# Kernel optimization log

Hardware: AMD Instinct MI355X
Metric: run time of the kernel (lower is better)

## Reference

```python
import jax, jax.numpy as jnp
import numpy as np

N = 100000      # num_entities
D = 128         # embedding_dim
H = 128         # hidden_layer_size
R2 = 100        # num_relations * 2 (with inverse relations)
B = 4           # num_bases
E = 400000      # num_edges


def setup_inputs() -> dict:
    key = jax.random.key(0)
    ks = jax.random.split(key, 12)
    s = 0.1
    return {
        "edge_index": jax.random.randint(ks[0], (2, E), 0, N),
        "edge_type": jax.random.randint(ks[1], (E,), 0, R2),
        "entity_embedding": jax.random.normal(ks[2], (N, D), jnp.float32) * s,
        "entity_embedding_bias": jnp.zeros((1, D), jnp.float32),
        "bases1": jax.random.normal(ks[3], (B, D, H), jnp.float32) * s,
        "comp1": jax.random.normal(ks[4], (R2, B), jnp.float32) * s,
        "root1": jax.random.normal(ks[5], (D, H), jnp.float32) * s,
        "bias1": jnp.zeros((H,), jnp.float32),
        "bases2": jax.random.normal(ks[6], (B, H, D), jnp.float32) * s,
        "comp2": jax.random.normal(ks[7], (R2, B), jnp.float32) * s,
        "root2": jax.random.normal(ks[8], (H, D), jnp.float32) * s,
        "bias2": jnp.zeros((D,), jnp.float32),
        "rel_emb": jax.random.normal(ks[9], (R2, D), jnp.float32) * s,
    }


def _rgcn_layer(x, bases, comp, root, bias, src, dst, et, norm):
    # gather source features and project through all bases: [E, B, out]
    xb = jnp.einsum('ei,bio->ebo', x[src], bases)
    # relation-specific basis mix per edge: [E, out]
    msg = jnp.einsum('eb,ebo->eo', comp[et], xb) * norm[:, None]
    # scatter-add aggregate to destination nodes
    agg = jax.ops.segment_sum(msg, dst, num_segments=N)
    return agg + x @ root + bias


def reference(edge_index, edge_type, entity_embedding, entity_embedding_bias,
              bases1, comp1, root1, bias1, bases2, comp2, root2, bias2, rel_emb):
    src, dst = edge_index[0], edge_index[1]
    # schlichtkrull normalization: 1 / |{edges into dst with same relation}|
    key = dst * R2 + edge_type
    counts = jax.ops.segment_sum(jnp.ones((E,), jnp.float32), key, num_segments=N * R2)
    norm = 1.0 / jnp.maximum(counts[key], 1.0)

    x = jax.nn.relu(entity_embedding + entity_embedding_bias)
    x = _rgcn_layer(x, bases1, comp1, root1, bias1, src, dst, edge_type, norm)
    x = jax.nn.relu(x)
    x = _rgcn_layer(x, bases2, comp2, root2, bias2, src, dst, edge_type, norm)

    # DistMult decoder over triples (src, edge_type, dst)
    score = jnp.sum(x[src] * rel_emb[edge_type] * x[dst], axis=-1)  # [E]
    # L2 penalty on relation embeddings
    penalty = jnp.sum(rel_emb ** 2)
    return score, penalty
```

## Files before the change

kernel.cpp:

```cpp
#include <hip/hip_runtime.h>

#define N_NODES 100000
#define DIM     128
#define RR      100
#define NE      400000
#define NBLK    196
#define NPB     32

typedef float  floatx4 __attribute__((ext_vector_type(4)));
typedef float  floatx2 __attribute__((ext_vector_type(2)));
typedef __bf16 bf16x8  __attribute__((ext_vector_type(8)));

static __device__ __forceinline__ unsigned short f2b(float f) {
    union { float f; unsigned int i; } v; v.f = f;
    unsigned int u = v.i;
    unsigned int r = (u + 0x7fffu + ((u >> 16) & 1u)) >> 16;
    return (unsigned short)r;
}
static __device__ __forceinline__ float b2f(unsigned int u16) {
    union { unsigned int i; float f; } v; v.i = u16 << 16; return v.f;
}
static __device__ __forceinline__ unsigned packbf(float a, float b) {
    return (unsigned)f2b(a) | ((unsigned)f2b(b) << 16);
}

__global__ void k_deg(const int* __restrict__ dst, int* __restrict__ deg, int E) {
    int e = blockIdx.x * 256 + threadIdx.x;
    if (e < E) atomicAdd(&deg[dst[e]], 1);
}

__global__ void k_scan_block(const int* __restrict__ deg, int* __restrict__ bsum) {
    __shared__ int sm[256];
    int b = blockIdx.x, t = threadIdx.x;
    int i0 = b * 512 + 2 * t;
    int a = (i0     < N_NODES) ? deg[i0]     : 0;
    int c = (i0 + 1 < N_NODES) ? deg[i0 + 1] : 0;
    sm[t] = a + c;
    __syncthreads();
    for (int s = 128; s > 0; s >>= 1) { if (t < s) sm[t] += sm[t + s]; __syncthreads(); }
    if (t == 0) bsum[b] = sm[0];
}

__global__ void k_scan_top(const int* __restrict__ bsum, int* __restrict__ boff) {
    __shared__ int sm[256];
    int t = threadIdx.x;
    int v = (t < NBLK) ? bsum[t] : 0;
    sm[t] = v;
    __syncthreads();
    for (int s = 1; s < 256; s <<= 1) {
        int u = (t >= s) ? sm[t - s] : 0;
        __syncthreads();
        sm[t] += u;
        __syncthreads();
    }
    if (t < NBLK) boff[t] = sm[t] - v;
}

__global__ void k_scan_down(const int* __restrict__ deg, const int* __restrict__ boff,
                            int* __restrict__ off) {
    __shared__ int sm[256];
    int b = blockIdx.x, t = threadIdx.x;
    int i0 = b * 512 + 2 * t;
    int a = (i0     < N_NODES) ? deg[i0]     : 0;
    int c = (i0 + 1 < N_NODES) ? deg[i0 + 1] : 0;
    int ts = a + c;
    sm[t] = ts;
    __syncthreads();
    for (int s = 1; s < 256; s <<= 1) {
        int u = (t >= s) ? sm[t - s] : 0;
        __syncthreads();
        sm[t] += u;
        __syncthreads();
    }
    int base = boff[b] + (sm[t] - ts);
    if (i0     < N_NODES) off[i0]     = base;
    if (i0 + 1 < N_NODES) off[i0 + 1] = base + a;
    if (b == 0 && t == 0) off[N_NODES] = NE;
}

__global__ void k_scatter(const int* __restrict__ src, const int* __restrict__ dst,
                          const int* __restrict__ et, const int* __restrict__ off,
                          int* __restrict__ cursor, int4* __restrict__ edesc, int E) {
    int e = blockIdx.x * 256 + threadIdx.x;
    if (e >= E) return;
    int d = dst[e];
    int pos = off[d] + atomicAdd(&cursor[d], 1);
    edesc[pos] = make_int4(src[e], (et[e] << 19) | e, d, 0);
}

__global__ void k_norm2(const int* __restrict__ off, int4* __restrict__ edesc, int E) {
    int p = blockIdx.x * 256 + threadIdx.x;
    if (p >= E) return;
    int4 me = edesc[p];
    int myt = me.y >> 19;
    int p0 = off[me.z], p1 = off[me.z + 1];
    int c = 0;
    for (int j = p0; j < p1; ++j)
        c += ((((const int*)edesc)[4 * j + 1] >> 19) == myt) ? 1 : 0;
    ((int*)edesc)[4 * p + 3] = __float_as_int(1.0f / (float)c);
}

__global__ void k_pre(const float* __restrict__ ent, const float* __restrict__ entb,
                      const float* __restrict__ bases1, const float* __restrict__ root1,
                      const float* __restrict__ bases2, const float* __restrict__ root2,
                      const float* __restrict__ rel,
                      unsigned short* __restrict__ x1,
                      unsigned short* __restrict__ wt1, unsigned short* __restrict__ wt2,
                      unsigned short* __restrict__ relb, float* __restrict__ out,
                      int* __restrict__ deg, int* __restrict__ cursor) {
    int b = blockIdx.x, t = threadIdx.x;
    if (b < 50000) {
        int i = b * 256 + t;
        float v = ent[i] + entb[i & (DIM - 1)];
        x1[i] = f2b(v > 0.0f ? v : 0.0f);
    } else if (b < 50320) {
        int i = (b - 50000) * 256 + t;
        int m = i / 640, k = i - m * 640;
        float v1, v2;
        if (k < 512) {
            int bb = k >> 7, kin = k & 127;
            v1 = bases1[(bb * 128 + kin) * 128 + m];
            v2 = bases2[(bb * 128 + kin) * 128 + m];
        } else {
            int kin = k - 512;
            v1 = root1[kin * 128 + m];
            v2 = root2[kin * 128 + m];
        }
        wt1[i] = f2b(v1);
        wt2[i] = f2b(v2);
    } else if (b < 50370) {
        int i = (b - 50320) * 256 + t;
        relb[i] = f2b(rel[i]);
    } else if (b < 51152) {
        int j = (b - 50370) * 256 + t;
        if (j < N_NODES) deg[j] = 0;
        else if (j < 2 * N_NODES) cursor[j - N_NODES] = 0;
    } else {
        __shared__ float sm[256];
        float v = 0.0f;
        for (int i = t; i < RR * DIM; i += 256) { float x = rel[i]; v += x * x; }
        sm[t] = v;
        __syncthreads();
        for (int s = 128; s > 0; s >>= 1) {
            if (t < s) sm[t] += sm[t + s];
            __syncthreads();
        }
        if (t == 0) out[NE] = sm[0];
    }
}

#define ACC(A) { A[0] += (floatx2){w0, w0} * xv; \
                 A[1] += (floatx2){w1, w1} * xv; \
                 A[2] += (floatx2){w2, w2} * xv; \
                 A[3] += (floatx2){w3, w3} * xv; }

__global__ __launch_bounds__(512, 4) void k_fused(const unsigned short* __restrict__ X,
                                                  const int4* __restrict__ edesc,
                                                  const int* __restrict__ off,
                                                  const float* __restrict__ comp,
                                                  const unsigned short* __restrict__ WT,
                                                  const float* __restrict__ bias,
                                                  unsigned short* __restrict__ out,
                                                  int do_relu) {
    __shared__ __align__(16) unsigned short Sacc[4 * NPB * 128];
    __shared__ __align__(16) unsigned short Bs0[128 * 64];
    __shared__ __align__(16) unsigned short Bs1[128 * 64];
    __shared__ float4 Cs[RR];

    const int t = threadIdx.x, wid = t >> 6, lane = t & 63;
    const int rbase = blockIdx.x * NPB;

    if (t < RR) Cs[t] = ((const float4*)comp)[t];
    __syncthreads();

    {
        const int nbase = rbase + wid * 4;
        const int lo = off[nbase], hi = off[nbase + 4];
        floatx2 a0[4], a1[4], a2[4], a3[4];
#pragma unroll
        for (int c = 0; c < 4; ++c) {
            a0[c] = (floatx2)0.0f; a1[c] = (floatx2)0.0f;
            a2[c] = (floatx2)0.0f; a3[c] = (floatx2)0.0f;
        }
        for (int base = lo; base < hi; base += 16) {
            int cnt = hi - base; if (cnt > 16) cnt = 16;
            int4 md = edesc[base + (lane & 15)];
            unsigned xp[16];
#pragma unroll
            for (int u = 0; u < 16; ++u) {
                int jc = (u < cnt) ? u : 0;
                int s = (int)__builtin_amdgcn_readlane((unsigned)md.x, (unsigned)jc);
                xp[u] = *(const unsigned*)(X + (size_t)s * 128 + 2 * lane);
            }
#pragma unroll
            for (int u = 0; u < 16; ++u) {
                if (u < cnt) {
                    int row = (int)__builtin_amdgcn_readlane((unsigned)md.z, (unsigned)u) - nbase;
                    int tt  = (int)__builtin_amdgcn_readlane((unsigned)md.y, (unsigned)u) >> 19;
                    float w = __int_as_float(__builtin_amdgcn_readlane((unsigned)md.w, (unsigned)u));
                    float4 cc = Cs[tt];
                    floatx2 xv = {b2f(xp[u] & 0xffffu), b2f(xp[u] >> 16)};
                    float w0 = w * cc.x, w1 = w * cc.y, w2 = w * cc.z, w3 = w * cc.w;
                    if      (row == 0) ACC(a0)
                    else if (row == 1) ACC(a1)
                    else if (row == 2) ACC(a2)
                    else               ACC(a3)
                }
            }
        }
        const int sw16 = lane >> 2, wo = 2 * (lane & 3);
#pragma unroll
        for (int r = 0; r < 4; ++r) {
            int R = wid * 4 + r;
            unsigned bo = (unsigned)(R * 128 + ((sw16 ^ (R & 15)) << 3) + wo);
            floatx2* A = (r == 0) ? a0 : (r == 1) ? a1 : (r == 2) ? a2 : a3;
#pragma unroll
            for (int c = 0; c < 4; ++c)
                *(unsigned*)(Sacc + c * (NPB * 128) + bo) = packbf(A[c].x, A[c].y);
        }
    }

    const int quad = lane >> 4, lr = lane & 15;
    const int wr = wid & 1, wc = wid >> 1;

    const int srow0 = t >> 3,        sg0 = t & 7;
    const int srow1 = 64 + (t >> 3), sg1 = t & 7;
    const unsigned bo0 = (unsigned)(srow0 * 64 + ((sg0 ^ (srow0 & 7)) << 3));
    const unsigned bo1 = (unsigned)(srow1 * 64 + ((sg1 ^ (srow1 & 7)) << 3));

    uint4 p0 = *(const uint4*)(WT + (size_t)srow0 * 640 + sg0 * 8);
    uint4 p1 = *(const uint4*)(WT + (size_t)srow1 * 640 + sg1 * 8);

    bf16x8 ax[4];
    {
        int grow = rbase + wr * 16 + lr;
#pragma unroll
        for (int ks = 0; ks < 4; ++ks)
            ax[ks] = *(const bf16x8*)(X + (size_t)grow * 128 + ks * 32 + quad * 8);
    }

    floatx4 acc[2];
    acc[0] = (floatx4)0.0f; acc[1] = (floatx4)0.0f;

    *(uint4*)(Bs0 + bo0) = p0;
    *(uint4*)(Bs0 + bo1) = p1;
    __syncthreads();

#pragma unroll
    for (int c = 0; c < 10; ++c) {
        const unsigned short* Bcur = (c & 1) ? Bs1 : Bs0;
        unsigned short*      Bnext = (c & 1) ? Bs0 : Bs1;
        uint4 n0, n1;
        if (c < 9) {
            n0 = *(const uint4*)(WT + (size_t)srow0 * 640 + (c + 1) * 64 + sg0 * 8);
            n1 = *(const uint4*)(WT + (size_t)srow1 * 640 + (c + 1) * 64 + sg1 * 8);
        }
#pragma unroll
        for (int ks2 = 0; ks2 < 2; ++ks2) {
            int ks = (c & 1) * 2 + ks2;
            bf16x8 a, b0, b1;
            int R = wr * 16 + lr;
            if (c < 8) {
                int ch = ((ks * 4 + quad) ^ (R & 15)) << 3;
                a = *(const bf16x8*)(Sacc + (c >> 1) * (NPB * 128) + R * 128 + ch);
            } else {
                a = ax[(c - 8) * 2 + ks2];
            }
            int g = ks2 * 4 + quad;
            int sch = (g ^ (lr & 7)) << 3;
            b0 = *(const bf16x8*)(Bcur + (wc * 32 + lr) * 64 + sch);
            b1 = *(const bf16x8*)(Bcur + (wc * 32 + 16 + lr) * 64 + sch);
            acc[0] = __builtin_amdgcn_mfma_f32_16x16x32_bf16(a, b0, acc[0], 0, 0, 0);
            acc[1] = __builtin_amdgcn_mfma_f32_16x16x32_bf16(a, b1, acc[1], 0, 0, 0);
        }
        if (c < 9) {
            *(uint4*)(Bnext + bo0) = n0;
            *(uint4*)(Bnext + bo1) = n1;
        }
        __syncthreads();
    }

#pragma unroll
    for (int reg = 0; reg < 4; ++reg) {
        int R = wr * 16 + quad * 4 + reg;
        int grow = rbase + R;
#pragma unroll
        for (int nj = 0; nj < 2; ++nj) {
            int n = wc * 32 + nj * 16 + lr;
            float v = acc[nj][reg] + bias[n];
            if (do_relu) v = v > 0.0f ? v : 0.0f;
            out[(size_t)grow * 128 + n] = f2b(v);
        }
    }
}

__global__ __launch_bounds__(256) void k_score(const unsigned short* __restrict__ xf,
                                               const int* __restrict__ src, const int* __restrict__ dst,
                                               const int* __restrict__ et,
                                               const unsigned short* __restrict__ relb,
                                               float* __restrict__ out, int E) {
    int g = threadIdx.x >> 4, li = threadIdx.x & 15;
    int e = blockIdx.x * 16 + g;
    if (e >= E) return;
    int s = src[e], d = dst[e], tt = et[e];
    uint4 au = *(const uint4*)(xf + (size_t)s * 128 + li * 8);
    uint4 bu = *(const uint4*)(xf + (size_t)d * 128 + li * 8);
    uint4 ru = *(const uint4*)(relb + (size_t)tt * 128 + li * 8);
    float v;
    v  = b2f(au.x & 0xffffu) * b2f(ru.x & 0xffffu) * b2f(bu.x & 0xffffu);
    v += b2f(au.x >> 16)     * b2f(ru.x >> 16)     * b2f(bu.x >> 16);
    v += b2f(au.y & 0xffffu) * b2f(ru.y & 0xffffu) * b2f(bu.y & 0xffffu);
    v += b2f(au.y >> 16)     * b2f(ru.y >> 16)     * b2f(bu.y >> 16);
    v += b2f(au.z & 0xffffu) * b2f(ru.z & 0xffffu) * b2f(bu.z & 0xffffu);
    v += b2f(au.z >> 16)     * b2f(ru.z >> 16)     * b2f(bu.z >> 16);
    v += b2f(au.w & 0xffffu) * b2f(ru.w & 0xffffu) * b2f(bu.w & 0xffffu);
    v += b2f(au.w >> 16)     * b2f(ru.w >> 16)     * b2f(bu.w >> 16);
    v += __shfl_xor(v, 8, 16);
    v += __shfl_xor(v, 4, 16);
    v += __shfl_xor(v, 2, 16);
    v += __shfl_xor(v, 1, 16);
    if (li == 0) out[e] = v;
}

extern "C" void kernel_launch(void* const* d_in, const int* in_sizes, int n_in,
                              void* d_out, int out_size, void* d_ws, size_t ws_size,
                              hipStream_t stream) {
    (void)in_sizes; (void)n_in; (void)out_size; (void)ws_size;
    const int* edge_index = (const int*)d_in[0];
    const int* edge_type  = (const int*)d_in[1];
    const float* ent    = (const float*)d_in[2];
    const float* entb   = (const float*)d_in[3];
    const float* bases1 = (const float*)d_in[4];
    const float* comp1  = (const float*)d_in[5];
    const float* root1  = (const float*)d_in[6];
    const float* bias1  = (const float*)d_in[7];
    const float* bases2 = (const float*)d_in[8];
    const float* comp2  = (const float*)d_in[9];
    const float* root2  = (const float*)d_in[10];
    const float* bias2  = (const float*)d_in[11];
    const float* rel    = (const float*)d_in[12];
    const int* src = edge_index;
    const int* dst = edge_index + NE;

    char* ws = (char*)d_ws;
    size_t off_b = 0;
    auto alloc = [&](size_t bytes) { void* p = ws + off_b; off_b = (off_b + bytes + 255) & ~(size_t)255; return p; };

    unsigned short* x1   = (unsigned short*)alloc((size_t)N_NODES * 128 * 2);
    unsigned short* x2   = (unsigned short*)alloc((size_t)N_NODES * 128 * 2);
    unsigned short* wt1  = (unsigned short*)alloc(128 * 640 * 2);
    unsigned short* wt2  = (unsigned short*)alloc(128 * 640 * 2);
    unsigned short* relb = (unsigned short*)alloc(RR * DIM * 2);
    int*   deg    = (int*)alloc((size_t)N_NODES * 4);
    int*   cursor = (int*)alloc((size_t)N_NODES * 4);
    int*   offv   = (int*)alloc((size_t)(N_NODES + 1) * 4);
    int*   bsum   = (int*)alloc(NBLK * 4);
    int*   boff   = (int*)alloc(NBLK * 4);
    int4*  edesc  = (int4*)alloc((size_t)(NE + 64) * 16);

    float* out = (float*)d_out;

    k_pre<<<51153, 256, 0, stream>>>(ent, entb, bases1, root1, bases2, root2, rel,
                                     x1, wt1, wt2, relb, out, deg, cursor);
    k_deg<<<(NE + 255) / 256, 256, 0, stream>>>(dst, deg, NE);
    k_scan_block<<<NBLK, 256, 0, stream>>>(deg, bsum);
    k_scan_top<<<1, 256, 0, stream>>>(bsum, boff);
    k_scan_down<<<NBLK, 256, 0, stream>>>(deg, boff, offv);
    k_scatter<<<(NE + 255) / 256, 256, 0, stream>>>(src, dst, edge_type, offv, cursor, edesc, NE);
    k_norm2<<<(NE + 255) / 256, 256, 0, stream>>>(offv, edesc, NE);

    int fgrid = N_NODES / NPB;
    k_fused<<<fgrid, 512, 0, stream>>>(x1, edesc, offv, comp1, wt1, bias1, x2, 1);
    k_fused<<<fgrid, 512, 0, stream>>>(x2, edesc, offv, comp2, wt2, bias2, x1, 0);
    k_score<<<(NE + 15) / 16, 256, 0, stream>>>(x1, src, dst, edge_type, relb, out, NE);
}
```

Baseline: 388.4 us.

## Split fused RGCN layer into message-gather and GEMM kernels with precomputed edge weights

Splits the fused aggregation+GEMM kernel in two. A gather kernel with 256-thread blocks writes per-node basis-mixed aggregates to a global bf16 buffer, and a GEMM kernel reads that buffer directly. Per-edge weights (norm times comp) are precomputed for both layers in k_norm2, which removes the shared comp table and per-edge multiplies from the gather loop. This frees LDS and lets the gather kernel run at higher occupancy, at the cost of an extra 100 MB global round trip per layer and two extra launches.

```diff
diff --git a/kernel.cpp b/kernel.cpp
--- a/kernel.cpp
+++ b/kernel.cpp
@@ -88,7 +88,9 @@
     edesc[pos] = make_int4(src[e], (et[e] << 19) | e, d, 0);
 }
 
-__global__ void k_norm2(const int* __restrict__ off, int4* __restrict__ edesc, int E) {
+__global__ void k_norm2(const int* __restrict__ off, const int4* __restrict__ edesc,
+                        const float4* __restrict__ comp1, const float4* __restrict__ comp2,
+                        float4* __restrict__ ew1, float4* __restrict__ ew2, int E) {
     int p = blockIdx.x * 256 + threadIdx.x;
     if (p >= E) return;
     int4 me = edesc[p];
@@ -97,7 +99,10 @@
     int c = 0;
     for (int j = p0; j < p1; ++j)
         c += ((((const int*)edesc)[4 * j + 1] >> 19) == myt) ? 1 : 0;
-    ((int*)edesc)[4 * p + 3] = __float_as_int(1.0f / (float)c);
+    float nrm = 1.0f / (float)c;
+    float4 c1 = comp1[myt], c2 = comp2[myt];
+    ew1[p] = make_float4(nrm * c1.x, nrm * c1.y, nrm * c1.z, nrm * c1.w);
+    ew2[p] = make_float4(nrm * c2.x, nrm * c2.y, nrm * c2.z, nrm * c2.w);
 }
 
 __global__ void k_pre(const float* __restrict__ ent, const float* __restrict__ entb,
@@ -154,72 +159,68 @@
                  A[2] += (floatx2){w2, w2} * xv; \
                  A[3] += (floatx2){w3, w3} * xv; }
 
-__global__ __launch_bounds__(512, 4) void k_fused(const unsigned short* __restrict__ X,
-                                                  const int4* __restrict__ edesc,
-                                                  const int* __restrict__ off,
-                                                  const float* __restrict__ comp,
-                                                  const unsigned short* __restrict__ WT,
-                                                  const float* __restrict__ bias,
-                                                  unsigned short* __restrict__ out,
-                                                  int do_relu) {
-    __shared__ __align__(16) unsigned short Sacc[4 * NPB * 128];
+__global__ __launch_bounds__(256) void k_msg(const unsigned short* __restrict__ X,
+                                             const int4* __restrict__ edesc,
+                                             const float4* __restrict__ ew,
+                                             const int* __restrict__ off,
+                                             unsigned short* __restrict__ Mg) {
+    const int t = threadIdx.x, lane = t & 63;
+    const int nbase = blockIdx.x * 16 + (t >> 6) * 4;
+    const int lo = off[nbase], hi = off[nbase + 4];
+    floatx2 a0[4], a1[4], a2[4], a3[4];
+#pragma unroll
+    for (int c = 0; c < 4; ++c) {
+        a0[c] = (floatx2)0.0f; a1[c] = (floatx2)0.0f;
+        a2[c] = (floatx2)0.0f; a3[c] = (floatx2)0.0f;
+    }
+    for (int base = lo; base < hi; base += 16) {
+        int cnt = hi - base; if (cnt > 16) cnt = 16;
+        int4   md = edesc[base + (lane & 15)];
+        float4 mw = ew[base + (lane & 15)];
+        unsigned xp[16];
+#pragma unroll
+        for (int u = 0; u < 16; ++u) {
+            int jc = (u < cnt) ? u : 0;
+            int s = (int)__builtin_amdgcn_readlane((unsigned)md.x, (unsigned)jc);
+            xp[u] = *(const unsigned*)(X + (size_t)s * 128 + 2 * lane);
+        }
+#pragma unroll
+        for (int u = 0; u < 16; ++u) {
+            if (u < cnt) {
+                int row = (int)__builtin_amdgcn_readlane((unsigned)md.z, (unsigned)u) - nbase;
+                float w0 = __int_as_float(__builtin_amdgcn_readlane(__float_as_uint(mw.x), (unsigned)u));
+                float w1 = __int_as_float(__builtin_amdgcn_readlane(__float_as_uint(mw.y), (unsigned)u));
+                float w2 = __int_as_float(__builtin_amdgcn_readlane(__float_as_uint(mw.z), (unsigned)u));
+                float w3 = __int_as_float(__builtin_amdgcn_readlane(__float_as_uint(mw.w), (unsigned)u));
+                floatx2 xv = {b2f(xp[u] & 0xffffu), b2f(xp[u] >> 16)};
+                if      (row == 0) ACC(a0)
+                else if (row == 1) ACC(a1)
+                else if (row == 2) ACC(a2)
+                else               ACC(a3)
+            }
+        }
+    }
+#pragma unroll
+    for (int r = 0; r < 4; ++r) {
+        floatx2* A = (r == 0) ? a0 : (r == 1) ? a1 : (r == 2) ? a2 : a3;
+#pragma unroll
+        for (int c = 0; c < 4; ++c)
+            *(unsigned*)(Mg + (size_t)(nbase + r) * 512 + c * 128 + 2 * lane) =
+                packbf(A[c].x, A[c].y);
+    }
+}
+
+__global__ __launch_bounds__(512, 4) void k_gemm(const unsigned short* __restrict__ X,
+                                                 const unsigned short* __restrict__ Mg,
+                                                 const unsigned short* __restrict__ WT,
+                                                 const float* __restrict__ bias,
+                                                 unsigned short* __restrict__ out,
+                                                 int do_relu) {
     __shared__ __align__(16) unsigned short Bs0[128 * 64];
     __shared__ __align__(16) unsigned short Bs1[128 * 64];
-    __shared__ float4 Cs[RR];
 
     const int t = threadIdx.x, wid = t >> 6, lane = t & 63;
     const int rbase = blockIdx.x * NPB;
-
-    if (t < RR) Cs[t] = ((const float4*)comp)[t];
-    __syncthreads();
-
-    {
-        const int nbase = rbase + wid * 4;
-        const int lo = off[nbase], hi = off[nbase + 4];
-        floatx2 a0[4], a1[4], a2[4], a3[4];
-#pragma unroll
-        for (int c = 0; c < 4; ++c) {
-            a0[c] = (floatx2)0.0f; a1[c] = (floatx2)0.0f;
-            a2[c] = (floatx2)0.0f; a3[c] = (floatx2)0.0f;
-        }
-        for (int base = lo; base < hi; base += 16) {
-            int cnt = hi - base; if (cnt > 16) cnt = 16;
-            int4 md = edesc[base + (lane & 15)];
-            unsigned xp[16];
-#pragma unroll
-            for (int u = 0; u < 16; ++u) {
-                int jc = (u < cnt) ? u : 0;
-                int s = (int)__builtin_amdgcn_readlane((unsigned)md.x, (unsigned)jc);
-                xp[u] = *(const unsigned*)(X + (size_t)s * 128 + 2 * lane);
-            }
-#pragma unroll
-            for (int u = 0; u < 16; ++u) {
-                if (u < cnt) {
-                    int row = (int)__builtin_amdgcn_readlane((unsigned)md.z, (unsigned)u) - nbase;
-                    int tt  = (int)__builtin_amdgcn_readlane((unsigned)md.y, (unsigned)u) >> 19;
-                    float w = __int_as_float(__builtin_amdgcn_readlane((unsigned)md.w, (unsigned)u));
-                    float4 cc = Cs[tt];
-                    floatx2 xv = {b2f(xp[u] & 0xffffu), b2f(xp[u] >> 16)};
-                    float w0 = w * cc.x, w1 = w * cc.y, w2 = w * cc.z, w3 = w * cc.w;
-                    if      (row == 0) ACC(a0)
-                    else if (row == 1) ACC(a1)
-                    else if (row == 2) ACC(a2)
-                    else               ACC(a3)
-                }
-            }
-        }
-        const int sw16 = lane >> 2, wo = 2 * (lane & 3);
-#pragma unroll
-        for (int r = 0; r < 4; ++r) {
-            int R = wid * 4 + r;
-            unsigned bo = (unsigned)(R * 128 + ((sw16 ^ (R & 15)) << 3) + wo);
-            floatx2* A = (r == 0) ? a0 : (r == 1) ? a1 : (r == 2) ? a2 : a3;
-#pragma unroll
-            for (int c = 0; c < 4; ++c)
-                *(unsigned*)(Sacc + c * (NPB * 128) + bo) = packbf(A[c].x, A[c].y);
-        }
-    }
-
     const int quad = lane >> 4, lr = lane & 15;
     const int wr = wid & 1, wc = wid >> 1;
 
@@ -245,6 +246,9 @@
     *(uint4*)(Bs0 + bo0) = p0;
     *(uint4*)(Bs0 + bo1) = p1;
     __syncthreads();
+
+    const int R = wr * 16 + lr;
+    const unsigned short* Arow = Mg + (size_t)(rbase + R) * 512;
 
 #pragma unroll
     for (int c = 0; c < 10; ++c) {
@@ -259,10 +263,8 @@
         for (int ks2 = 0; ks2 < 2; ++ks2) {
             int ks = (c & 1) * 2 + ks2;
             bf16x8 a, b0, b1;
-            int R = wr * 16 + lr;
             if (c < 8) {
-                int ch = ((ks * 4 + quad) ^ (R & 15)) << 3;
-                a = *(const bf16x8*)(Sacc + (c >> 1) * (NPB * 128) + R * 128 + ch);
+                a = *(const bf16x8*)(Arow + (c >> 1) * 128 + ks * 32 + quad * 8);
             } else {
                 a = ax[(c - 8) * 2 + ks2];
             }
@@ -282,8 +284,8 @@
 
 #pragma unroll
     for (int reg = 0; reg < 4; ++reg) {
-        int R = wr * 16 + quad * 4 + reg;
-        int grow = rbase + R;
+        int Ro = wr * 16 + quad * 4 + reg;
+        int grow = rbase + Ro;
 #pragma unroll
         for (int nj = 0; nj < 2; ++nj) {
             int n = wc * 32 + nj * 16 + lr;
@@ -348,6 +350,7 @@
 
     unsigned short* x1   = (unsigned short*)alloc((size_t)N_NODES * 128 * 2);
     unsigned short* x2   = (unsigned short*)alloc((size_t)N_NODES * 128 * 2);
+    unsigned short* Mg   = (unsigned short*)alloc((size_t)N_NODES * 512 * 2);
     unsigned short* wt1  = (unsigned short*)alloc(128 * 640 * 2);
     unsigned short* wt2  = (unsigned short*)alloc(128 * 640 * 2);
     unsigned short* relb = (unsigned short*)alloc(RR * DIM * 2);
@@ -357,6 +360,8 @@
     int*   bsum   = (int*)alloc(NBLK * 4);
     int*   boff   = (int*)alloc(NBLK * 4);
     int4*  edesc  = (int4*)alloc((size_t)(NE + 64) * 16);
+    float4* ew1   = (float4*)alloc((size_t)NE * 16);
+    float4* ew2   = (float4*)alloc((size_t)NE * 16);
 
     float* out = (float*)d_out;
 
@@ -367,10 +372,15 @@
     k_scan_top<<<1, 256, 0, stream>>>(bsum, boff);
     k_scan_down<<<NBLK, 256, 0, stream>>>(deg, boff, offv);
     k_scatter<<<(NE + 255) / 256, 256, 0, stream>>>(src, dst, edge_type, offv, cursor, edesc, NE);
-    k_norm2<<<(NE + 255) / 256, 256, 0, stream>>>(offv, edesc, NE);
-
-    int fgrid = N_NODES / NPB;
-    k_fused<<<fgrid, 512, 0, stream>>>(x1, edesc, offv, comp1, wt1, bias1, x2, 1);
-    k_fused<<<fgrid, 512, 0, stream>>>(x2, edesc, offv, comp2, wt2, bias2, x1, 0);
+    k_norm2<<<(NE + 255) / 256, 256, 0, stream>>>(offv, edesc,
+                                                  (const float4*)comp1, (const float4*)comp2,
+                                                  ew1, ew2, NE);
+
+    int mgrid = N_NODES / 16;
+    int ggrid = N_NODES / NPB;
+    k_msg <<<mgrid, 256, 0, stream>>>(x1, edesc, ew1, offv, Mg);
+    k_gemm<<<ggrid, 512, 0, stream>>>(x1, Mg, wt1, bias1, x2, 1);
+    k_msg <<<mgrid, 256, 0, stream>>>(x2, edesc, ew2, offv, Mg);
+    k_gemm<<<ggrid, 512, 0, stream>>>(x2, Mg, wt2, bias2, x1, 0);
     k_score<<<(NE + 15) / 16, 256, 0, stream>>>(x1, src, dst, edge_type, relb, out, NE);
 }
```

Result: slower. 487.0 us (+25.4%).
